# Kernel tuning notes

Hardware: AMD Instinct MI355X
Metric: run time of the kernel (lower is better)

## Reference

```python
import jax, jax.numpy as jnp
import numpy as np

B, N, D, P, K = 4, 2048, 512, 16, 4
EPS_BW = 1e-8
EPS_LN = 1e-5


def setup_inputs() -> dict:
    key = jax.random.key(0)
    ks = jax.random.split(key, 8)
    charge = jax.random.normal(ks[0], (B, N, D), dtype=jnp.float32)
    position = jax.random.normal(ks[1], (B, N, P), dtype=jnp.float32)
    mass = jax.random.uniform(ks[2], (B, N, 1), dtype=jnp.float32)
    # parameters
    log_bandwidth = jnp.zeros((K,), dtype=jnp.float32)
    W_charge = jax.random.normal(ks[3], (D * K, D), dtype=jnp.float32) / np.sqrt(D)   # torch Linear weight (out,in)
    W_combine = jax.random.normal(ks[4], (D, D * K), dtype=jnp.float32) / np.sqrt(D * K)
    gamma = jnp.ones((D,), dtype=jnp.float32)
    beta = jnp.zeros((D,), dtype=jnp.float32)
    return {"charge": charge, "position": position, "mass": mass,
            "log_bandwidth": log_bandwidth, "W_charge": W_charge,
            "W_combine": W_combine, "gamma": gamma, "beta": beta}


def reference(charge, position, mass, log_bandwidth, W_charge, W_combine, gamma, beta):
    # pairwise squared distances: (B, N, N)
    diff = position[:, :, None, :] - position[:, None, :, :]
    dist_sq = jnp.sum(diff * diff, axis=-1)
    # multi-bandwidth Gaussian kernels: (B, N, N, K)
    bandwidths = jnp.exp(log_bandwidth)
    kernels = jnp.exp(-dist_sq[..., None] / (2.0 * bandwidths + EPS_BW))
    # mass weighting: mass (B,N,1) -> (B,1,N,1), broadcast over query axis and kernels
    weighted_kernels = kernels * mass[:, None, :, :]
    # project charges: (B, N, K, D)
    projected = (charge @ W_charge.T).reshape(B, N, K, D)
    # aggregate over neighbours j: field[b,i,k,d] = sum_j wk[b,i,j,k] * proj[b,j,k,d]
    field = jnp.einsum('bijk,bjkd->bikd', weighted_kernels, projected)
    field = field.reshape(B, N, K * D) @ W_combine.T  # (B, N, D)
    # LayerNorm
    mean = jnp.mean(field, axis=-1, keepdims=True)
    var = jnp.var(field, axis=-1, keepdims=True)
    normed = (field - mean) * jax.lax.rsqrt(var + EPS_LN)
    return normed * gamma + beta
```

## Files before the change

### kernel.cpp

```cpp
#include <hip/hip_runtime.h>


typedef __bf16 bf16x8 __attribute__((ext_vector_type(8)));
typedef float f32x4 __attribute__((ext_vector_type(4)));

__device__ __forceinline__ unsigned short f2bf(float f) {
    unsigned u = __float_as_uint(f);
    unsigned r = (u + 0x7fffu + ((u >> 16) & 1u)) >> 16;
    return (unsigned short)r;
}
__device__ __forceinline__ float bf2f(unsigned short h) {
    return __uint_as_float(((unsigned)h) << 16);
}
__device__ __forceinline__ void g2l16(const unsigned short* g, unsigned short* l) {
    __builtin_amdgcn_global_load_lds(
        (const __attribute__((address_space(1))) unsigned int*)g,
        (__attribute__((address_space(3))) unsigned int*)l, 16, 0, 0);
}

__global__ __launch_bounds__(256) void k0_all(const float* __restrict__ charge,
                                              const float* __restrict__ Wc,
                                              const float* __restrict__ pos,
                                              unsigned short* __restrict__ ch16,
                                              unsigned short* __restrict__ wc16,
                                              unsigned short* __restrict__ posA,
                                              unsigned short* __restrict__ posB1,
                                              unsigned short* __restrict__ posB2,
                                              float* __restrict__ rsq)
{
    const int bx = blockIdx.x, tid = threadIdx.x;
    if (bx < 5120) {
        const float* src = (bx < 4096) ? charge : Wc;
        unsigned short* dst = (bx < 4096) ? ch16 : wc16;
        size_t i = (size_t)(bx < 4096 ? bx : bx - 4096) * 256 + tid;
        float4 v = reinterpret_cast<const float4*>(src)[i];
        unsigned short o[4] = {f2bf(v.x), f2bf(v.y), f2bf(v.z), f2bf(v.w)};
        reinterpret_cast<uint2*>(dst)[i] = *reinterpret_cast<uint2*>(&o[0]);
        return;
    }
    const int row = (bx - 5120) * 256 + tid;
    const float* src = &pos[(size_t)row * 16];
    float p[16];
#pragma unroll
    for (int cc = 0; cc < 4; cc++) {
        float4 v = *reinterpret_cast<const float4*>(&src[cc * 4]);
        p[cc * 4 + 0] = v.x; p[cc * 4 + 1] = v.y; p[cc * 4 + 2] = v.z; p[cc * 4 + 3] = v.w;
    }
    float r = 0.f;
    unsigned short h[16], lo[16], z[8] = {0, 0, 0, 0, 0, 0, 0, 0};
#pragma unroll
    for (int d = 0; d < 16; d++) {
        r = __builtin_fmaf(p[d], p[d], r);
        h[d] = f2bf(p[d]);
        lo[d] = f2bf(p[d] - bf2f(h[d]));
    }
    rsq[row] = r;
    size_t o = (size_t)row * 32;
    *reinterpret_cast<int4*>(&posA[o + 0])   = *reinterpret_cast<int4*>(&h[0]);
    *reinterpret_cast<int4*>(&posA[o + 8])   = *reinterpret_cast<int4*>(&h[8]);
    *reinterpret_cast<int4*>(&posA[o + 16])  = *reinterpret_cast<int4*>(&lo[0]);
    *reinterpret_cast<int4*>(&posA[o + 24])  = *reinterpret_cast<int4*>(&lo[8]);
    *reinterpret_cast<int4*>(&posB1[o + 0])  = *reinterpret_cast<int4*>(&h[0]);
    *reinterpret_cast<int4*>(&posB1[o + 8])  = *reinterpret_cast<int4*>(&h[8]);
    *reinterpret_cast<int4*>(&posB1[o + 16]) = *reinterpret_cast<int4*>(&h[0]);
    *reinterpret_cast<int4*>(&posB1[o + 24]) = *reinterpret_cast<int4*>(&h[8]);
    *reinterpret_cast<int4*>(&posB2[o + 0])  = *reinterpret_cast<int4*>(&lo[0]);
    *reinterpret_cast<int4*>(&posB2[o + 8])  = *reinterpret_cast<int4*>(&lo[8]);
    *reinterpret_cast<int4*>(&posB2[o + 16]) = *reinterpret_cast<int4*>(&z[0]);
    *reinterpret_cast<int4*>(&posB2[o + 24]) = *reinterpret_cast<int4*>(&z[0]);
}

__global__ __launch_bounds__(256) void k0_cvt(const float* __restrict__ src,
                                              unsigned short* __restrict__ dst)
{
    size_t i = (size_t)blockIdx.x * 256 + threadIdx.x;
    float4 v = reinterpret_cast<const float4*>(src)[i];
    unsigned short o[4] = {f2bf(v.x), f2bf(v.y), f2bf(v.z), f2bf(v.w)};
    reinterpret_cast<uint2*>(dst)[i] = *reinterpret_cast<uint2*>(&o[0]);
}

__global__ __launch_bounds__(256, 3) void k1_proj(const unsigned short* __restrict__ wc16,
                                                  const unsigned short* __restrict__ ch16,
                                                  const float* __restrict__ mass,
                                                  unsigned short* __restrict__ projm_t)
{
    __shared__ alignas(16) unsigned short As[2][128 * 32];
    __shared__ alignas(16) unsigned short Bs[2][128 * 32];
    const int tid = threadIdx.x, lane = tid & 63, wid = tid >> 6;
    const int q = lane >> 4, l15 = lane & 15;
    const int sw = (l15 >> 2) & 3;
    const int m0 = blockIdx.y * 128, n0 = blockIdx.x * 128;
    const int wm = (wid & 1) * 64, wn = (wid >> 1) * 64;

    f32x4 acc[4][4];
#pragma unroll
    for (int i = 0; i < 4; i++)
#pragma unroll
        for (int j = 0; j < 4; j++) acc[i][j] = (f32x4){0.f, 0.f, 0.f, 0.f};

    const int w = tid & 255;
    (void)w;

#pragma unroll
    for (int q4 = 0; q4 < 4; q4++) {
        int chunk = q4 * 256 + tid;
        int ww = chunk & 511, row = ww >> 2;
        int gc4 = (ww & 3) ^ ((ww >> 4) & 3);
        if (chunk < 512)
            g2l16(&wc16[(size_t)(m0 + row) * 512 + gc4 * 8], &As[0][ww * 8]);
        else
            g2l16(&ch16[(size_t)(n0 + row) * 512 + gc4 * 8], &Bs[0][ww * 8]);
    }
    __syncthreads();

    for (int n = 0; n < 16; n++) {
        const int p = n & 1;
        const int k1 = (n + 1) * 32;
        if (k1 < 512) {
#pragma unroll
            for (int q4 = 0; q4 < 4; q4++) {
                int chunk = q4 * 256 + tid;
                int ww = chunk & 511, row = ww >> 2;
                int gc4 = (ww & 3) ^ ((ww >> 4) & 3);
                if (chunk < 512)
                    g2l16(&wc16[(size_t)(m0 + row) * 512 + k1 + gc4 * 8], &As[p ^ 1][ww * 8]);
                else
                    g2l16(&ch16[(size_t)(n0 + row) * 512 + k1 + gc4 * 8], &Bs[p ^ 1][ww * 8]);
            }
        }
        bf16x8 af[4], bfr[4];
#pragma unroll
        for (int it = 0; it < 4; it++)
            af[it] = *reinterpret_cast<const bf16x8*>(&As[p][(wm + it * 16 + l15) * 32 + (q ^ sw) * 8]);
#pragma unroll
        for (int ct = 0; ct < 4; ct++)
            bfr[ct] = *reinterpret_cast<const bf16x8*>(&Bs[p][(wn + ct * 16 + l15) * 32 + (q ^ sw) * 8]);
#pragma unroll
        for (int it = 0; it < 4; it++)
#pragma unroll
            for (int ct = 0; ct < 4; ct++)
                acc[it][ct] = __builtin_amdgcn_mfma_f32_16x16x32_bf16(af[it], bfr[ct], acc[it][ct], 0, 0, 0);
        __syncthreads();
    }
#pragma unroll
    for (int ct = 0; ct < 4; ct++) {
        int nn = n0 + wn + ct * 16 + l15;
        float mf = mass[nn];
#pragma unroll
        for (int it = 0; it < 4; it++) {
            int mrow = m0 + wm + it * 16 + q * 4;
#pragma unroll
            for (int r = 0; r < 4; r++)
                projm_t[(size_t)(mrow + r) * 8192 + nn] = f2bf(acc[it][ct][r] * mf);
        }
    }
}

__global__ __launch_bounds__(256, 2) void k2_field(const unsigned short* __restrict__ posA,
                                                   const unsigned short* __restrict__ posB1,
                                                   const unsigned short* __restrict__ posB2,
                                                   const float* __restrict__ rsq,
                                                   const float* __restrict__ logbw,
                                                   const unsigned short* __restrict__ projm_t,
                                                   unsigned short* __restrict__ field)
{
    __shared__ alignas(16) unsigned short Bs[3][256 * 32];
    __shared__ alignas(16) unsigned short Wl[2][128 * 40];

    const int tid = threadIdx.x, lane = tid & 63, wid = tid >> 6;
    const int q = lane >> 4, l15 = lane & 15;
    const int sw = (l15 >> 2) & 3;
    const int L = blockIdx.x;
    const int xcd = L & 7, idx = L >> 3;
    const int i_t = idx & 15, cb = xcd * 4 + (idx >> 4);
    const int c0 = (cb & 7) * 256, b = cb >> 3;
    const int i0 = i_t * 128;
    const int kb = c0 >> 9;
    const float bw = __expf(logbw[kb]);
    const float s2 = -1.4426950408889634f / (2.0f * bw + 1e-8f);
    const float c2 = -2.0f * s2;
    const int bN = b * 2048;

    bf16x8 afG[2];
    float riS2[2][4];
#pragma unroll
    for (int t = 0; t < 2; t++) {
        afG[t] = *reinterpret_cast<const bf16x8*>(
            &posA[(size_t)(bN + i0 + wid * 32 + t * 16 + l15) * 32 + q * 8]);
#pragma unroll
        for (int r = 0; r < 4; r++)
            riS2[t][r] = rsq[bN + i0 + wid * 32 + t * 16 + q * 4 + r] * s2;
    }

    const int wo_i = (wid >> 1) * 64, wo_c = (wid & 1) * 128;
    const size_t gbase = (size_t)c0 * 8192 + bN;

    f32x4 acc[4][8];
#pragma unroll
    for (int i = 0; i < 4; i++)
#pragma unroll
        for (int j = 0; j < 8; j++) acc[i][j] = (f32x4){0.f, 0.f, 0.f, 0.f};

#pragma unroll
    for (int q4 = 0; q4 < 4; q4++) {
        int chunk = q4 * 256 + tid;
        int row = chunk >> 2, gc4 = (chunk & 3) ^ ((chunk >> 4) & 3);
        g2l16(&projm_t[gbase + (size_t)row * 8192 + gc4 * 8], &Bs[0][chunk * 8]);
    }

    int bs_r = 0;
    for (int n = 0; n < 64; n++) {
        const int j0 = n * 32;
        const int p = n & 1;
        bf16x8 gb1[2], gb2[2];
        float rj2[2];
#pragma unroll
        for (int jt2 = 0; jt2 < 2; jt2++) {
            int j = bN + j0 + jt2 * 16 + l15;
            gb1[jt2] = *reinterpret_cast<const bf16x8*>(&posB1[(size_t)j * 32 + q * 8]);
            gb2[jt2] = *reinterpret_cast<const bf16x8*>(&posB2[(size_t)j * 32 + q * 8]);
            rj2[jt2] = rsq[j] * s2;
        }
        if (j0 + 32 < 2048) {
            const int bs_w = bs_r + 1 == 3 ? 0 : bs_r + 1;
            const size_t gb = gbase + j0 + 32;
#pragma unroll
            for (int q4 = 0; q4 < 4; q4++) {
                int chunk = q4 * 256 + tid;
                int row = chunk >> 2, gc4 = (chunk & 3) ^ ((chunk >> 4) & 3);
                g2l16(&projm_t[gb + (size_t)row * 8192 + gc4 * 8], &Bs[bs_w][chunk * 8]);
            }
        }
#pragma unroll
        for (int jt2 = 0; jt2 < 2; jt2++) {
#pragma unroll
            for (int t = 0; t < 2; t++) {
                f32x4 g = (f32x4){0.f, 0.f, 0.f, 0.f};
                g = __builtin_amdgcn_mfma_f32_16x16x32_bf16(afG[t], gb2[jt2], g, 0, 0, 0);
                g = __builtin_amdgcn_mfma_f32_16x16x32_bf16(afG[t], gb1[jt2], g, 0, 0, 0);
#pragma unroll
                for (int r = 0; r < 4; r++) {
                    float x = __builtin_fmaf(g[r], c2, riS2[t][r] + rj2[jt2]);
                    Wl[p][(wid * 32 + t * 16 + q * 4 + r) * 40 + jt2 * 16 + l15] =
                        f2bf(__builtin_amdgcn_exp2f(x));
                }
            }
        }
        __syncthreads();
        bf16x8 af[4], bfr[8];
#pragma unroll
        for (int it = 0; it < 4; it++)
            af[it] = *reinterpret_cast<const bf16x8*>(&Wl[p][(wo_i + it * 16 + l15) * 40 + q * 8]);
#pragma unroll
        for (int ct = 0; ct < 8; ct++)
            bfr[ct] = *reinterpret_cast<const bf16x8*>(&Bs[bs_r][(wo_c + ct * 16 + l15) * 32 + (q ^ sw) * 8]);
#pragma unroll
        for (int it = 0; it < 4; it++)
#pragma unroll
            for (int ct = 0; ct < 8; ct++)
                acc[it][ct] = __builtin_amdgcn_mfma_f32_16x16x32_bf16(af[it], bfr[ct], acc[it][ct], 0, 0, 0);
        bs_r = bs_r + 1 == 3 ? 0 : bs_r + 1;
    }
#pragma unroll
    for (int it = 0; it < 4; it++) {
#pragma unroll
        for (int ct = 0; ct < 8; ct++) {
            int gi = bN + i0 + wo_i + it * 16 + q * 4;
            int gc = c0 + wo_c + ct * 16 + l15;
#pragma unroll
            for (int r = 0; r < 4; r++)
                field[(size_t)(gi + r) * 2048 + gc] = f2bf(acc[it][ct][r]);
        }
    }
}

__global__ __launch_bounds__(256, 3) void k3_combine(const unsigned short* __restrict__ field,
                                                     const unsigned short* __restrict__ wcb16,
                                                     float* __restrict__ out)
{
    __shared__ alignas(16) unsigned short As[2][64 * 32];
    __shared__ alignas(16) unsigned short Bs[2][128 * 32];
    const int tid = threadIdx.x, lane = tid & 63, wid = tid >> 6;
    const int q = lane >> 4, l15 = lane & 15;
    const int sw = (l15 >> 2) & 3;
    const int m0 = blockIdx.y * 64, n0 = blockIdx.x * 128;
    const int wn = wid * 32;

    f32x4 acc[4][2];
#pragma unroll
    for (int i = 0; i < 4; i++)
#pragma unroll
        for (int j = 0; j < 2; j++) acc[i][j] = (f32x4){0.f, 0.f, 0.f, 0.f};

#pragma unroll
    for (int q3 = 0; q3 < 3; q3++) {
        int chunk = q3 * 256 + tid;
        if (chunk < 256) {
            int row = chunk >> 2, gc4 = (chunk & 3) ^ ((chunk >> 4) & 3);
            g2l16(&field[(size_t)(m0 + row) * 2048 + gc4 * 8], &As[0][chunk * 8]);
        } else {
            int ww = chunk - 256, row = ww >> 2, gc4 = (ww & 3) ^ ((ww >> 4) & 3);
            g2l16(&wcb16[(size_t)(n0 + row) * 2048 + gc4 * 8], &Bs[0][ww * 8]);
        }
    }
    __syncthreads();

    for (int n = 0; n < 64; n++) {
        const int p = n & 1;
        const int k1 = (n + 1) * 32;
        if (k1 < 2048) {
#pragma unroll
            for (int q3 = 0; q3 < 3; q3++) {
                int chunk = q3 * 256 + tid;
                if (chunk < 256) {
                    int row = chunk >> 2, gc4 = (chunk & 3) ^ ((chunk >> 4) & 3);
                    g2l16(&field[(size_t)(m0 + row) * 2048 + k1 + gc4 * 8], &As[p ^ 1][chunk * 8]);
                } else {
                    int ww = chunk - 256, row = ww >> 2, gc4 = (ww & 3) ^ ((ww >> 4) & 3);
                    g2l16(&wcb16[(size_t)(n0 + row) * 2048 + k1 + gc4 * 8], &Bs[p ^ 1][ww * 8]);
                }
            }
        }
        bf16x8 af[4], bfr[2];
#pragma unroll
        for (int it = 0; it < 4; it++)
            af[it] = *reinterpret_cast<const bf16x8*>(&As[p][(it * 16 + l15) * 32 + (q ^ sw) * 8]);
#pragma unroll
        for (int ct = 0; ct < 2; ct++)
            bfr[ct] = *reinterpret_cast<const bf16x8*>(&Bs[p][(wn + ct * 16 + l15) * 32 + (q ^ sw) * 8]);
#pragma unroll
        for (int it = 0; it < 4; it++)
#pragma unroll
            for (int ct = 0; ct < 2; ct++)
                acc[it][ct] = __builtin_amdgcn_mfma_f32_16x16x32_bf16(af[it], bfr[ct], acc[it][ct], 0, 0, 0);
        __syncthreads();
    }
#pragma unroll
    for (int it = 0; it < 4; it++) {
#pragma unroll
        for (int ct = 0; ct < 2; ct++) {
            int m = m0 + it * 16 + q * 4;
            int nn = n0 + wn + ct * 16 + l15;
#pragma unroll
            for (int r = 0; r < 4; r++)
                out[(size_t)(m + r) * 512 + nn] = acc[it][ct][r];
        }
    }
}

__global__ __launch_bounds__(256) void k4_ln(float* __restrict__ out,
                                             const float* __restrict__ gamma,
                                             const float* __restrict__ beta)
{
    __shared__ float red[8];
    const int row = blockIdx.x, tid = threadIdx.x;
    float2 x = *reinterpret_cast<const float2*>(&out[(size_t)row * 512 + tid * 2]);
    float s = x.x + x.y;
    float ss = x.x * x.x + x.y * x.y;
#pragma unroll
    for (int off = 32; off > 0; off >>= 1) {
        s += __shfl_down(s, off);
        ss += __shfl_down(ss, off);
    }
    int wid = tid >> 6;
    if ((tid & 63) == 0) { red[wid * 2] = s; red[wid * 2 + 1] = ss; }
    __syncthreads();
    s = red[0] + red[2] + red[4] + red[6];
    ss = red[1] + red[3] + red[5] + red[7];
    float mean = s * (1.f / 512.f);
    float var = ss * (1.f / 512.f) - mean * mean;
    float inv = rsqrtf(var + 1e-5f);
    float g0 = gamma[tid * 2], g1 = gamma[tid * 2 + 1];
    float b0 = beta[tid * 2], b1 = beta[tid * 2 + 1];
    float2 o;
    o.x = (x.x - mean) * inv * g0 + b0;
    o.y = (x.y - mean) * inv * g1 + b1;
    *reinterpret_cast<float2*>(&out[(size_t)row * 512 + tid * 2]) = o;
}

extern "C" void kernel_launch(void* const* d_in, const int* in_sizes, int n_in,
                              void* d_out, int out_size, void* d_ws, size_t ws_size,
                              hipStream_t stream)
{
    const float* charge   = (const float*)d_in[0];
    const float* position = (const float*)d_in[1];
    const float* mass     = (const float*)d_in[2];
    const float* logbw    = (const float*)d_in[3];
    const float* Wc       = (const float*)d_in[4];
    const float* Wcb      = (const float*)d_in[5];
    const float* gamma    = (const float*)d_in[6];
    const float* beta     = (const float*)d_in[7];

    unsigned short* projm_t = (unsigned short*)d_ws;
    unsigned short* field   = projm_t + (size_t)2048 * 8192;
    unsigned short* wcb16   = projm_t;
    unsigned short* ch16    = field;
    unsigned short* wc16    = field + (size_t)8192 * 512;
    unsigned short* posA  = (unsigned short*)d_out;
    unsigned short* posB1 = posA + (size_t)8192 * 32;
    unsigned short* posB2 = posB1 + (size_t)8192 * 32;
    float* rsq = (float*)(posB2 + (size_t)8192 * 32);
    float* out = (float*)d_out;

    k0_all<<<5152, 256, 0, stream>>>(charge, Wc, position, ch16, wc16, posA, posB1, posB2, rsq);
    k1_proj<<<dim3(64, 16), 256, 0, stream>>>(wc16, ch16, mass, projm_t);
    k2_field<<<512, 256, 0, stream>>>(posA, posB1, posB2, rsq, logbw, projm_t, field);
    k0_cvt<<<1024, 256, 0, stream>>>(Wcb, wcb16);
    k3_combine<<<dim3(4, 128), 256, 0, stream>>>(field, wcb16, out);
    k4_ln<<<8192, 256, 0, stream>>>(out, gamma, beta);
}
```

Measured before the change: 263.1 us.

## Restructure barriers and prefetch in field and combine GEMMs, deepen combine K-tile

In the projection and field kernels the single __syncthreads moves to the top of each iteration, so the next tile's async LDS loads are issued after the barrier. The field kernel drops from a triple-buffered to a double-buffered projm tile. It also prefetches the next step's position and rsq operands in registers and computes the distance with two independent MFMAs instead of chaining them. The combine kernel doubles its K tile to 64 with an 8-way XOR swizzle, halving the barrier count at the cost of more LDS per block.

```diff
diff --git a/kernel.cpp b/kernel.cpp
--- a/kernel.cpp
+++ b/kernel.cpp
@@ -98,9 +98,6 @@
 #pragma unroll
         for (int j = 0; j < 4; j++) acc[i][j] = (f32x4){0.f, 0.f, 0.f, 0.f};
 
-    const int w = tid & 255;
-    (void)w;
-
 #pragma unroll
     for (int q4 = 0; q4 < 4; q4++) {
         int chunk = q4 * 256 + tid;
@@ -111,10 +108,10 @@
         else
             g2l16(&ch16[(size_t)(n0 + row) * 512 + gc4 * 8], &Bs[0][ww * 8]);
     }
-    __syncthreads();
 
     for (int n = 0; n < 16; n++) {
         const int p = n & 1;
+        __syncthreads();
         const int k1 = (n + 1) * 32;
         if (k1 < 512) {
 #pragma unroll
@@ -140,7 +137,6 @@
 #pragma unroll
             for (int ct = 0; ct < 4; ct++)
                 acc[it][ct] = __builtin_amdgcn_mfma_f32_16x16x32_bf16(af[it], bfr[ct], acc[it][ct], 0, 0, 0);
-        __syncthreads();
     }
 #pragma unroll
     for (int ct = 0; ct < 4; ct++) {
@@ -164,7 +160,7 @@
                                                    const unsigned short* __restrict__ projm_t,
                                                    unsigned short* __restrict__ field)
 {
-    __shared__ alignas(16) unsigned short Bs[3][256 * 32];
+    __shared__ alignas(16) unsigned short Bs[2][256 * 32];
     __shared__ alignas(16) unsigned short Wl[2][128 * 40];
 
     const int tid = threadIdx.x, lane = tid & 63, wid = tid >> 6;
@@ -201,6 +197,15 @@
 #pragma unroll
         for (int j = 0; j < 8; j++) acc[i][j] = (f32x4){0.f, 0.f, 0.f, 0.f};
 
+    bf16x8 gb1[2], gb2[2];
+    float rj2[2];
+#pragma unroll
+    for (int jt2 = 0; jt2 < 2; jt2++) {
+        int j = bN + jt2 * 16 + l15;
+        gb1[jt2] = *reinterpret_cast<const bf16x8*>(&posB1[(size_t)j * 32 + q * 8]);
+        gb2[jt2] = *reinterpret_cast<const bf16x8*>(&posB2[(size_t)j * 32 + q * 8]);
+        rj2[jt2] = rsq[j] * s2;
+    }
 #pragma unroll
     for (int q4 = 0; q4 < 4; q4++) {
         int chunk = q4 * 256 + tid;
@@ -208,58 +213,53 @@
         g2l16(&projm_t[gbase + (size_t)row * 8192 + gc4 * 8], &Bs[0][chunk * 8]);
     }
 
-    int bs_r = 0;
     for (int n = 0; n < 64; n++) {
-        const int j0 = n * 32;
         const int p = n & 1;
-        bf16x8 gb1[2], gb2[2];
-        float rj2[2];
 #pragma unroll
         for (int jt2 = 0; jt2 < 2; jt2++) {
-            int j = bN + j0 + jt2 * 16 + l15;
-            gb1[jt2] = *reinterpret_cast<const bf16x8*>(&posB1[(size_t)j * 32 + q * 8]);
-            gb2[jt2] = *reinterpret_cast<const bf16x8*>(&posB2[(size_t)j * 32 + q * 8]);
-            rj2[jt2] = rsq[j] * s2;
-        }
-        if (j0 + 32 < 2048) {
-            const int bs_w = bs_r + 1 == 3 ? 0 : bs_r + 1;
-            const size_t gb = gbase + j0 + 32;
+#pragma unroll
+            for (int t = 0; t < 2; t++) {
+                f32x4 z = (f32x4){0.f, 0.f, 0.f, 0.f};
+                f32x4 g1 = __builtin_amdgcn_mfma_f32_16x16x32_bf16(afG[t], gb1[jt2], z, 0, 0, 0);
+                f32x4 g2 = __builtin_amdgcn_mfma_f32_16x16x32_bf16(afG[t], gb2[jt2], z, 0, 0, 0);
+#pragma unroll
+                for (int r = 0; r < 4; r++) {
+                    float x = __builtin_fmaf(g1[r] + g2[r], c2, riS2[t][r] + rj2[jt2]);
+                    Wl[p][(wid * 32 + t * 16 + q * 4 + r) * 40 + jt2 * 16 + l15] =
+                        f2bf(__builtin_amdgcn_exp2f(x));
+                }
+            }
+        }
+        __syncthreads();
+        if (n + 1 < 64) {
+            const int j0n = (n + 1) * 32;
+#pragma unroll
+            for (int jt2 = 0; jt2 < 2; jt2++) {
+                int j = bN + j0n + jt2 * 16 + l15;
+                gb1[jt2] = *reinterpret_cast<const bf16x8*>(&posB1[(size_t)j * 32 + q * 8]);
+                gb2[jt2] = *reinterpret_cast<const bf16x8*>(&posB2[(size_t)j * 32 + q * 8]);
+                rj2[jt2] = rsq[j] * s2;
+            }
+            const size_t gb = gbase + j0n;
 #pragma unroll
             for (int q4 = 0; q4 < 4; q4++) {
                 int chunk = q4 * 256 + tid;
                 int row = chunk >> 2, gc4 = (chunk & 3) ^ ((chunk >> 4) & 3);
-                g2l16(&projm_t[gb + (size_t)row * 8192 + gc4 * 8], &Bs[bs_w][chunk * 8]);
-            }
-        }
-#pragma unroll
-        for (int jt2 = 0; jt2 < 2; jt2++) {
-#pragma unroll
-            for (int t = 0; t < 2; t++) {
-                f32x4 g = (f32x4){0.f, 0.f, 0.f, 0.f};
-                g = __builtin_amdgcn_mfma_f32_16x16x32_bf16(afG[t], gb2[jt2], g, 0, 0, 0);
-                g = __builtin_amdgcn_mfma_f32_16x16x32_bf16(afG[t], gb1[jt2], g, 0, 0, 0);
-#pragma unroll
-                for (int r = 0; r < 4; r++) {
-                    float x = __builtin_fmaf(g[r], c2, riS2[t][r] + rj2[jt2]);
-                    Wl[p][(wid * 32 + t * 16 + q * 4 + r) * 40 + jt2 * 16 + l15] =
-                        f2bf(__builtin_amdgcn_exp2f(x));
-                }
-            }
-        }
-        __syncthreads();
+                g2l16(&projm_t[gb + (size_t)row * 8192 + gc4 * 8], &Bs[p ^ 1][chunk * 8]);
+            }
+        }
         bf16x8 af[4], bfr[8];
 #pragma unroll
         for (int it = 0; it < 4; it++)
             af[it] = *reinterpret_cast<const bf16x8*>(&Wl[p][(wo_i + it * 16 + l15) * 40 + q * 8]);
 #pragma unroll
         for (int ct = 0; ct < 8; ct++)
-            bfr[ct] = *reinterpret_cast<const bf16x8*>(&Bs[bs_r][(wo_c + ct * 16 + l15) * 32 + (q ^ sw) * 8]);
+            bfr[ct] = *reinterpret_cast<const bf16x8*>(&Bs[p][(wo_c + ct * 16 + l15) * 32 + (q ^ sw) * 8]);
 #pragma unroll
         for (int it = 0; it < 4; it++)
 #pragma unroll
             for (int ct = 0; ct < 8; ct++)
                 acc[it][ct] = __builtin_amdgcn_mfma_f32_16x16x32_bf16(af[it], bfr[ct], acc[it][ct], 0, 0, 0);
-        bs_r = bs_r + 1 == 3 ? 0 : bs_r + 1;
     }
 #pragma unroll
     for (int it = 0; it < 4; it++) {
@@ -278,11 +278,10 @@
                                                      const unsigned short* __restrict__ wcb16,
                                                      float* __restrict__ out)
 {
-    __shared__ alignas(16) unsigned short As[2][64 * 32];
-    __shared__ alignas(16) unsigned short Bs[2][128 * 32];
+    __shared__ alignas(16) unsigned short As[2][64 * 64];
+    __shared__ alignas(16) unsigned short Bs[2][128 * 64];
     const int tid = threadIdx.x, lane = tid & 63, wid = tid >> 6;
     const int q = lane >> 4, l15 = lane & 15;
-    const int sw = (l15 >> 2) & 3;
     const int m0 = blockIdx.y * 64, n0 = blockIdx.x * 128;
     const int wn = wid * 32;
 
@@ -293,47 +292,59 @@
         for (int j = 0; j < 2; j++) acc[i][j] = (f32x4){0.f, 0.f, 0.f, 0.f};
 
 #pragma unroll
-    for (int q3 = 0; q3 < 3; q3++) {
-        int chunk = q3 * 256 + tid;
-        if (chunk < 256) {
-            int row = chunk >> 2, gc4 = (chunk & 3) ^ ((chunk >> 4) & 3);
-            g2l16(&field[(size_t)(m0 + row) * 2048 + gc4 * 8], &As[0][chunk * 8]);
+    for (int q6 = 0; q6 < 6; q6++) {
+        int chunk = q6 * 256 + tid;
+        if (chunk < 512) {
+            int row = chunk >> 3, lc = chunk & 7;
+            g2l16(&field[(size_t)(m0 + row) * 2048 + ((lc ^ (row & 7)) * 8)],
+                  &As[0][chunk * 8]);
         } else {
-            int ww = chunk - 256, row = ww >> 2, gc4 = (ww & 3) ^ ((ww >> 4) & 3);
-            g2l16(&wcb16[(size_t)(n0 + row) * 2048 + gc4 * 8], &Bs[0][ww * 8]);
-        }
-    }
-    __syncthreads();
-
-    for (int n = 0; n < 64; n++) {
+            int w = chunk - 512, row = w >> 3, lc = w & 7;
+            g2l16(&wcb16[(size_t)(n0 + row) * 2048 + ((lc ^ (row & 7)) * 8)],
+                  &Bs[0][w * 8]);
+        }
+    }
+
+    for (int n = 0; n < 32; n++) {
         const int p = n & 1;
-        const int k1 = (n + 1) * 32;
+        __syncthreads();
+        const int k1 = (n + 1) * 64;
         if (k1 < 2048) {
 #pragma unroll
-            for (int q3 = 0; q3 < 3; q3++) {
-                int chunk = q3 * 256 + tid;
-                if (chunk < 256) {
-                    int row = chunk >> 2, gc4 = (chunk & 3) ^ ((chunk >> 4) & 3);
-                    g2l16(&field[(size_t)(m0 + row) * 2048 + k1 + gc4 * 8], &As[p ^ 1][chunk * 8]);
+            for (int q6 = 0; q6 < 6; q6++) {
+                int chunk = q6 * 256 + tid;
+                if (chunk < 512) {
+                    int row = chunk >> 3, lc = chunk & 7;
+                    g2l16(&field[(size_t)(m0 + row) * 2048 + k1 + ((lc ^ (row & 7)) * 8)],
+                          &As[p ^ 1][chunk * 8]);
                 } else {
-                    int ww = chunk - 256, row = ww >> 2, gc4 = (ww & 3) ^ ((ww >> 4) & 3);
-                    g2l16(&wcb16[(size_t)(n0 + row) * 2048 + k1 + gc4 * 8], &Bs[p ^ 1][ww * 8]);
+                    int w = chunk - 512, row = w >> 3, lc = w & 7;
+                    g2l16(&wcb16[(size_t)(n0 + row) * 2048 + k1 + ((lc ^ (row & 7)) * 8)],
+                          &Bs[p ^ 1][w * 8]);
                 }
             }
         }
-        bf16x8 af[4], bfr[2];
-#pragma unroll
-        for (int it = 0; it < 4; it++)
-            af[it] = *reinterpret_cast<const bf16x8*>(&As[p][(it * 16 + l15) * 32 + (q ^ sw) * 8]);
-#pragma unroll
-        for (int ct = 0; ct < 2; ct++)
-            bfr[ct] = *reinterpret_cast<const bf16x8*>(&Bs[p][(wn + ct * 16 + l15) * 32 + (q ^ sw) * 8]);
-#pragma unroll
-        for (int it = 0; it < 4; it++)
-#pragma unroll
-            for (int ct = 0; ct < 2; ct++)
-                acc[it][ct] = __builtin_amdgcn_mfma_f32_16x16x32_bf16(af[it], bfr[ct], acc[it][ct], 0, 0, 0);
-        __syncthreads();
+#pragma unroll
+        for (int kk = 0; kk < 2; kk++) {
+            bf16x8 af[4], bfr[2];
+#pragma unroll
+            for (int it = 0; it < 4; it++) {
+                int row = it * 16 + l15;
+                af[it] = *reinterpret_cast<const bf16x8*>(
+                    &As[p][row * 64 + (((kk * 4 + q) ^ (row & 7)) * 8)]);
+            }
+#pragma unroll
+            for (int ct = 0; ct < 2; ct++) {
+                int row = wn + ct * 16 + l15;
+                bfr[ct] = *reinterpret_cast<const bf16x8*>(
+                    &Bs[p][row * 64 + (((kk * 4 + q) ^ (row & 7)) * 8)]);
+            }
+#pragma unroll
+            for (int it = 0; it < 4; it++)
+#pragma unroll
+                for (int ct = 0; ct < 2; ct++)
+                    acc[it][ct] = __builtin_amdgcn_mfma_f32_16x16x32_bf16(af[it], bfr[ct], acc[it][ct], 0, 0, 0);
+        }
     }
 #pragma unroll
     for (int it = 0; it < 4; it++) {
```

Result: slower. 271.1 us (+3.1%).
